# Optimization experiments

Measured on AMD Instinct MI355X. Metric: run time of the kernel, lower is better.

Reference implementation:

```python
import jax, jax.numpy as jnp
import numpy as np

B, T, H, NSPK = 8, 1024, 1024, 2
LN_EPS = 1e-5


def setup_inputs() -> dict:
    key = jax.random.key(0)
    ks = jax.random.split(key, 12)
    s = 1.0 / np.sqrt(H)
    return {
        "x": jax.random.normal(ks[0], (B, T, H), jnp.float32),
        "qmask": jax.random.uniform(ks[1], (B, T, NSPK), jnp.float32),
        "dia_len": jax.random.randint(ks[2], (B,), T // 2, T + 1),
        "wp": 8,
        "wf": 8,
        "W_msg": jax.random.normal(ks[3], (H, H), jnp.float32) * s,
        "b_msg": jax.random.normal(ks[4], (H,), jnp.float32) * s,
        "W_self": jax.random.normal(ks[5], (H, H), jnp.float32) * s,
        "b_self": jax.random.normal(ks[6], (H,), jnp.float32) * s,
        "W_out": jax.random.normal(ks[7], (H, H), jnp.float32) * s,
        "b_out": jax.random.normal(ks[8], (H,), jnp.float32) * s,
        "gamma": jnp.ones((H,), jnp.float32),
        "beta": jnp.zeros((H,), jnp.float32),
    }


def reference(x, qmask, dia_len, wp, wf, W_msg, b_msg, W_self, b_self, W_out, b_out, gamma, beta):
    Bb, Tt, Hh = x.shape
    spk = jnp.argmax(qmask, axis=-1)                     # [B,T]
    pos = jnp.arange(Tt)
    offs = jnp.arange(-wp, wf + 1)                       # [W]
    idx = pos[:, None] + offs[None, :]                   # [T,W] window indices
    vlen = dia_len[:, None, None]                        # [B,1,1]
    valid = (idx[None] >= 0) & (idx[None] <= vlen - 1)   # [B,T,W]
    idxc = jnp.clip(idx, 0, Tt - 1)
    nb = jnp.take(x, idxc, axis=1)                       # [B,T,W,H]
    nb_spk = jnp.take(spk, idxc, axis=1)                 # [B,T,W]
    same = (nb_spk == spk[:, :, None]).astype(x.dtype)
    w = jnp.where(valid, 0.5 + 0.5 * same, 0.0)          # speaker weights, masked
    cnt = jnp.maximum(valid.sum(-1).astype(x.dtype), 1.0)  # window sizes [B,T]
    msg = jnp.einsum('btw,btwh->bth', w, nb) / cnt[..., None]
    h = x @ W_self + b_self + msg @ W_msg + b_msg        # per-node fusion
    node_valid = (pos[None, :] < dia_len[:, None])[..., None]
    out = jnp.where(node_valid, h, x)                    # nodes past dia_len keep x
    y = jax.nn.relu(out) @ W_out + b_out                 # dropout = identity (eval)
    z = x + y
    mean = z.mean(-1, keepdims=True)
    var = z.var(-1, keepdims=True)
    return gamma * (z - mean) / jnp.sqrt(var + LN_EPS) + beta
```

## Files before the change

### kernel.cpp

```cpp
#include <hip/hip_runtime.h>


typedef unsigned short u16;
typedef float floatx4 __attribute__((ext_vector_type(4)));
typedef short shortx8 __attribute__((ext_vector_type(8)));

#define T_ 1024
#define H_ 1024

__device__ __forceinline__ float bf2f(u16 v) {
    return __uint_as_float(((unsigned)v) << 16);
}
__device__ __forceinline__ u16 f2bf(float f) {
    unsigned u = __float_as_uint(f);
    return (u16)((u + 0x7fffu + ((u >> 16) & 1u)) >> 16);
}
__device__ __forceinline__ void async16(const void* g, void* l) {
    __builtin_amdgcn_global_load_lds(
        (__attribute__((address_space(1))) void*)g,
        (__attribute__((address_space(3))) void*)l, 16, 0, 0);
}

__global__ __launch_bounds__(256)
void prep(const float* __restrict__ Wself, const float* __restrict__ Wmsg,
          const float* __restrict__ Wout, const float* __restrict__ x,
          u16* __restrict__ wt1, u16* __restrict__ wt_out, u16* __restrict__ xbf)
{
    __shared__ float s[32][33];
    const int bid = blockIdx.x;
    if (bid < 3072) {
        const int wid = bid >> 10;
        const int rem = bid & 1023;
        const float* src = (wid == 0) ? Wself : ((wid == 1) ? Wmsg : Wout);
        const int n0 = (rem & 31) * 32, k0 = (rem >> 5) * 32;
        const int tx = threadIdx.x & 31, ty = threadIdx.x >> 5;
#pragma unroll
        for (int i = 0; i < 4; ++i) {
            int k = k0 + ty + 8 * i;
            s[ty + 8 * i][tx] = src[(size_t)k * H_ + n0 + tx];
        }
        __syncthreads();
#pragma unroll
        for (int i = 0; i < 4; ++i) {
            int n = n0 + ty + 8 * i;
            u16 v = f2bf(s[tx][ty + 8 * i]);
            if (wid == 0)      wt1[(size_t)n * 1024 + k0 + tx] = v;
            else if (wid == 1) wt1[(size_t)(n + 1024) * 1024 + k0 + tx] = v;
            else               wt_out[(size_t)n * 1024 + k0 + tx] = v;
        }
    } else {
        const size_t i = ((size_t)(bid - 3072) * 256 + threadIdx.x) * 8;
        float4 v0 = *(const float4*)(x + i);
        float4 v1 = *(const float4*)(x + i + 4);
        ushort4 o0, o1;
        o0.x = f2bf(v0.x); o0.y = f2bf(v0.y); o0.z = f2bf(v0.z); o0.w = f2bf(v0.w);
        o1.x = f2bf(v1.x); o1.y = f2bf(v1.y); o1.z = f2bf(v1.z); o1.w = f2bf(v1.w);
        *(ushort4*)(xbf + i) = o0;
        *(ushort4*)(xbf + i + 4) = o1;
    }
}

template <int KLEN, int EPI>
__global__ __launch_bounds__(256)
void gemm_bt(const u16* __restrict__ A, const u16* __restrict__ Bt,
             u16* __restrict__ O0, u16* __restrict__ O1)
{
    __shared__ u16 smem[2 * 8192];
    const int tid = threadIdx.x;
    const int bn = blockIdx.x * 128;
    const int bm = blockIdx.y * 128;
    const int kb = blockIdx.z * KLEN;
    const int wave = tid >> 6, lane = tid & 63;
    const int wr = wave >> 1, wc = wave & 1;
    const int lrow = lane & 15, lq = lane >> 4;

    const int srow = tid >> 2;
    const int skc  = (tid & 3) ^ ((srow >> 1) & 3);
    const u16* gA0 = A + (size_t)(bm + srow) * 1024 + kb + skc * 8;
    const u16* gA1 = gA0 + (size_t)64 * 1024;
    const u16* gB0 = Bt + (size_t)(bn + srow) * 1024 + kb + skc * 8;
    const u16* gB1 = gB0 + (size_t)64 * 1024;

    floatx4 acc[4][4];
#pragma unroll
    for (int i = 0; i < 4; ++i)
#pragma unroll
        for (int j = 0; j < 4; ++j)
            acc[i][j] = (floatx4){0.f, 0.f, 0.f, 0.f};

    const int swz = (lrow >> 1) & 3;
    const int aoff = (wr * 64 + lrow) * 32 + ((lq ^ swz) * 8);
    const int boff = 4096 + (wc * 64 + lrow) * 32 + ((lq ^ swz) * 8);

    auto issue = [&](int s, int p) {
        u16* base = smem + p * 8192 + wave * 512;
        const int k = s * 32;
        async16(gA0 + k, base);
        async16(gA1 + k, base + 2048);
        async16(gB0 + k, base + 4096);
        async16(gB1 + k, base + 4096 + 2048);
    };

    constexpr int NS = KLEN / 32;
    issue(0, 0);
#pragma unroll 2
    for (int s = 0; s < NS; ++s) {
        const int p = s & 1;
        if (s + 1 < NS) {
            issue(s + 1, p ^ 1);
            asm volatile("s_waitcnt vmcnt(4)" ::: "memory");
        } else {
            asm volatile("s_waitcnt vmcnt(0)" ::: "memory");
        }
        asm volatile("s_barrier" ::: "memory");
        const u16* pa = smem + p * 8192 + aoff;
        const u16* pb = smem + p * 8192 + boff;
        shortx8 av[4], bv[4];
#pragma unroll
        for (int i = 0; i < 4; ++i) av[i] = *(const shortx8*)(pa + i * 512);
#pragma unroll
        for (int j = 0; j < 4; ++j) bv[j] = *(const shortx8*)(pb + j * 512);
#pragma unroll
        for (int i = 0; i < 4; ++i)
#pragma unroll
            for (int j = 0; j < 4; ++j)
                acc[i][j] = __builtin_amdgcn_mfma_f32_16x16x32_bf16(
                    av[i], bv[j], acc[i][j], 0, 0, 0);
        asm volatile("s_barrier" ::: "memory");
    }

    u16* O;
    int cbase;
    if (EPI == 0) { O = (bn < 1024) ? O0 : O1; cbase = bn & 1023; }
    else          { O = blockIdx.z ? O1 : O0;  cbase = bn; }
#pragma unroll
    for (int i = 0; i < 4; ++i) {
        const int row0 = bm + wr * 64 + i * 16 + lq * 4;
#pragma unroll
        for (int j = 0; j < 4; ++j) {
            const int col = cbase + wc * 64 + j * 16 + lrow;
#pragma unroll
            for (int r = 0; r < 4; ++r)
                O[(size_t)(row0 + r) * 1024 + col] = f2bf(acc[i][j][r]);
        }
    }
}

__global__ __launch_bounds__(256)
void combine(u16* __restrict__ uv, const u16* __restrict__ v,
             const float* __restrict__ x, const float* __restrict__ qmask,
             const int* __restrict__ dia_len, const float* __restrict__ b_self,
             const float* __restrict__ b_msg)
{
    const int t = blockIdx.x;
    const int b = blockIdx.y;
    const int tid = threadIdx.x;
    const int dlen = dia_len[b];
    const int c4 = tid * 4;
    const size_t rowg = (size_t)b * T_ + t;

    const float* qb = qmask + (size_t)b * T_ * 2;
    const int spk_t = (qb[t * 2 + 1] > qb[t * 2]) ? 1 : 0;

    float wts[17];
    int cnt = 0;
#pragma unroll
    for (int o = 0; o < 17; ++o) {
        const int idx = t + o - 8;
        if (idx >= 0 && idx < dlen) {
            ++cnt;
            const int spk_i = (qb[idx * 2 + 1] > qb[idx * 2]) ? 1 : 0;
            wts[o] = (spk_i == spk_t) ? 1.0f : 0.5f;
        } else {
            wts[o] = 0.0f;
        }
    }
    const float inv = 1.0f / (float)(cnt > 0 ? cnt : 1);

    float a0 = 0.f, a1 = 0.f, a2 = 0.f, a3 = 0.f;
#pragma unroll
    for (int o = 0; o < 17; ++o) {
        if (wts[o] != 0.0f) {
            const float w = wts[o] * inv;
            ushort4 vv = *(const ushort4*)(v + (rowg + (o - 8)) * 1024 + c4);
            a0 += w * bf2f(vv.x); a1 += w * bf2f(vv.y);
            a2 += w * bf2f(vv.z); a3 += w * bf2f(vv.w);
        }
    }

    float4 bs;
    {
        float4 b1 = *(const float4*)(b_self + c4);
        float4 b2 = *(const float4*)(b_msg + c4);
        bs.x = b1.x + b2.x; bs.y = b1.y + b2.y;
        bs.z = b1.z + b2.z; bs.w = b1.w + b2.w;
    }

    ushort4 u4 = *(const ushort4*)(uv + rowg * 1024 + c4);
    float4 xv = *(const float4*)(x + rowg * H_ + c4);
    const bool sel = (t < dlen);
    float h0 = bf2f(u4.x) + bs.x + a0;
    float h1 = bf2f(u4.y) + bs.y + a1;
    float h2 = bf2f(u4.z) + bs.z + a2;
    float h3 = bf2f(u4.w) + bs.w + a3;
    ushort4 outv;
    outv.x = f2bf(fmaxf(sel ? h0 : xv.x, 0.f));
    outv.y = f2bf(fmaxf(sel ? h1 : xv.y, 0.f));
    outv.z = f2bf(fmaxf(sel ? h2 : xv.z, 0.f));
    outv.w = f2bf(fmaxf(sel ? h3 : xv.w, 0.f));
    *(ushort4*)(uv + rowg * 1024 + c4) = outv;
}

__global__ __launch_bounds__(256)
void ln_final(const u16* __restrict__ P0, const u16* __restrict__ P1,
              const float* __restrict__ x, const float* __restrict__ b_out,
              const float* __restrict__ gamma, const float* __restrict__ beta,
              float* __restrict__ out)
{
    const int row = blockIdx.x;
    const int tid = threadIdx.x;
    const size_t base = (size_t)row * H_ + tid * 4;
    float4 xv = *(const float4*)(x + base);
    ushort4 p0 = *(const ushort4*)(P0 + base);
    ushort4 p1 = *(const ushort4*)(P1 + base);
    float4 bo = *(const float4*)(b_out + tid * 4);
    float4 v;
    v.x = xv.x + bf2f(p0.x) + bf2f(p1.x) + bo.x;
    v.y = xv.y + bf2f(p0.y) + bf2f(p1.y) + bo.y;
    v.z = xv.z + bf2f(p0.z) + bf2f(p1.z) + bo.z;
    v.w = xv.w + bf2f(p0.w) + bf2f(p1.w) + bo.w;
    float s = v.x + v.y + v.z + v.w;
    float q = v.x * v.x + v.y * v.y + v.z * v.z + v.w * v.w;
#pragma unroll
    for (int off = 32; off > 0; off >>= 1) {
        s += __shfl_down(s, off);
        q += __shfl_down(q, off);
    }
    __shared__ float ps[4], pq[4];
    const int wave = tid >> 6, lane = tid & 63;
    if (lane == 0) { ps[wave] = s; pq[wave] = q; }
    __syncthreads();
    const float S = ps[0] + ps[1] + ps[2] + ps[3];
    const float Q = pq[0] + pq[1] + pq[2] + pq[3];
    const float mean = S * (1.0f / 1024.0f);
    const float var = Q * (1.0f / 1024.0f) - mean * mean;
    const float inv = rsqrtf(var + 1e-5f);
    float4 g = *(const float4*)(gamma + tid * 4);
    float4 bt = *(const float4*)(beta + tid * 4);
    float4 o;
    o.x = g.x * (v.x - mean) * inv + bt.x;
    o.y = g.y * (v.y - mean) * inv + bt.y;
    o.z = g.z * (v.z - mean) * inv + bt.z;
    o.w = g.w * (v.w - mean) * inv + bt.w;
    *(float4*)(out + base) = o;
}

extern "C" void kernel_launch(void* const* d_in, const int* in_sizes, int n_in,
                              void* d_out, int out_size, void* d_ws, size_t ws_size,
                              hipStream_t stream)
{
    (void)in_sizes; (void)n_in; (void)out_size; (void)ws_size;
    const float* x       = (const float*)d_in[0];
    const float* qmask   = (const float*)d_in[1];
    const int*   dia_len = (const int*)d_in[2];
    const float* W_msg   = (const float*)d_in[5];
    const float* b_msg   = (const float*)d_in[6];
    const float* W_self  = (const float*)d_in[7];
    const float* b_self  = (const float*)d_in[8];
    const float* W_out   = (const float*)d_in[9];
    const float* b_out   = (const float*)d_in[10];
    const float* gamma   = (const float*)d_in[11];
    const float* beta    = (const float*)d_in[12];
    float* out = (float*)d_out;

    char* ws = (char*)d_ws;
    u16* region0 = (u16*)ws;
    u16* region1 = (u16*)(ws + (size_t)(16u << 20));
    u16* region2 = (u16*)(ws + (size_t)(32u << 20));
    u16* wt1     = (u16*)(ws + (size_t)(48u << 20));
    u16* wt_out  = (u16*)(ws + (size_t)(52u << 20));

    prep<<<dim3(7168), 256, 0, stream>>>(W_self, W_msg, W_out, x,
                                         wt1, wt_out, region0);
    gemm_bt<1024, 0><<<dim3(16, 64, 1), 256, 0, stream>>>(region0, wt1,
                                                          region1, region2);
    combine<<<dim3(T_, 8), 256, 0, stream>>>(region1, region2, x, qmask,
                                             dia_len, b_self, b_msg);
    gemm_bt<512, 1><<<dim3(8, 64, 2), 256, 0, stream>>>(region1, wt_out,
                                                        region2, region0);
    ln_final<<<dim3(8192), 256, 0, stream>>>(region2, region0, x, b_out,
                                             gamma, beta, out);
}
```

Baseline: 229.6 us.

## Use 32x32x16 MFMA with triple-buffered LDS and bf16 x in combine

The GEMM switches from 16x16x32 to 32x32x16 bf16 MFMA tiles (2x2 per wave) with new LDS offsets and output mapping. It moves to a three-stage LDS ring, which lets it drop the trailing barrier in each k-step. Separately, combine reads the bf16 copy of x instead of the fp32 x for rows past dia_len, halving that read traffic. The bf16 read adds rounding only on that passthrough path, which is fed to a bf16 output anyway. The single remaining barrier with a 3-buffer ring is meant to stay race-free because a buffer is only refilled two steps after it is read.

Measured after the change: 231.9 us. Within noise of the previous version (+1.0%).

```diff
diff --git a/kernel.cpp b/kernel.cpp
--- a/kernel.cpp
+++ b/kernel.cpp
@@ -2,7 +2,7 @@
 
 
 typedef unsigned short u16;
-typedef float floatx4 __attribute__((ext_vector_type(4)));
+typedef float floatx16 __attribute__((ext_vector_type(16)));
 typedef short shortx8 __attribute__((ext_vector_type(8)));
 
 #define T_ 1024
@@ -65,14 +65,14 @@
 void gemm_bt(const u16* __restrict__ A, const u16* __restrict__ Bt,
              u16* __restrict__ O0, u16* __restrict__ O1)
 {
-    __shared__ u16 smem[2 * 8192];
+    __shared__ u16 smem[3 * 8192];
     const int tid = threadIdx.x;
     const int bn = blockIdx.x * 128;
     const int bm = blockIdx.y * 128;
     const int kb = blockIdx.z * KLEN;
     const int wave = tid >> 6, lane = tid & 63;
     const int wr = wave >> 1, wc = wave & 1;
-    const int lrow = lane & 15, lq = lane >> 4;
+    const int l32 = lane & 31, hi = lane >> 5;
 
     const int srow = tid >> 2;
     const int skc  = (tid & 3) ^ ((srow >> 1) & 3);
@@ -81,19 +81,29 @@
     const u16* gB0 = Bt + (size_t)(bn + srow) * 1024 + kb + skc * 8;
     const u16* gB1 = gB0 + (size_t)64 * 1024;
 
-    floatx4 acc[4][4];
-#pragma unroll
-    for (int i = 0; i < 4; ++i)
-#pragma unroll
-        for (int j = 0; j < 4; ++j)
-            acc[i][j] = (floatx4){0.f, 0.f, 0.f, 0.f};
-
-    const int swz = (lrow >> 1) & 3;
-    const int aoff = (wr * 64 + lrow) * 32 + ((lq ^ swz) * 8);
-    const int boff = 4096 + (wc * 64 + lrow) * 32 + ((lq ^ swz) * 8);
-
-    auto issue = [&](int s, int p) {
-        u16* base = smem + p * 8192 + wave * 512;
+    floatx16 acc[2][2];
+#pragma unroll
+    for (int i = 0; i < 2; ++i)
+#pragma unroll
+        for (int j = 0; j < 2; ++j)
+#pragma unroll
+            for (int r = 0; r < 16; ++r)
+                acc[i][j][r] = 0.f;
+
+    int offA[2][2], offB[2][2];
+#pragma unroll
+    for (int i = 0; i < 2; ++i) {
+        const int rowA = wr * 64 + i * 32 + l32;
+        const int rowB = wc * 64 + i * 32 + l32;
+#pragma unroll
+        for (int s2 = 0; s2 < 2; ++s2) {
+            offA[i][s2] = rowA * 32 + (((2 * s2 + hi) ^ ((rowA >> 1) & 3)) * 8);
+            offB[i][s2] = 4096 + rowB * 32 + (((2 * s2 + hi) ^ ((rowB >> 1) & 3)) * 8);
+        }
+    }
+
+    auto issue = [&](int s, int q) {
+        u16* base = smem + q * 8192 + wave * 512;
         const int k = s * 32;
         async16(gA0 + k, base);
         async16(gA1 + k, base + 2048);
@@ -103,30 +113,34 @@
 
     constexpr int NS = KLEN / 32;
     issue(0, 0);
-#pragma unroll 2
+    int qr = 0;
     for (int s = 0; s < NS; ++s) {
-        const int p = s & 1;
         if (s + 1 < NS) {
-            issue(s + 1, p ^ 1);
+            const int qw = (qr == 2) ? 0 : qr + 1;
+            issue(s + 1, qw);
             asm volatile("s_waitcnt vmcnt(4)" ::: "memory");
         } else {
             asm volatile("s_waitcnt vmcnt(0)" ::: "memory");
         }
         asm volatile("s_barrier" ::: "memory");
-        const u16* pa = smem + p * 8192 + aoff;
-        const u16* pb = smem + p * 8192 + boff;
-        shortx8 av[4], bv[4];
-#pragma unroll
-        for (int i = 0; i < 4; ++i) av[i] = *(const shortx8*)(pa + i * 512);
-#pragma unroll
-        for (int j = 0; j < 4; ++j) bv[j] = *(const shortx8*)(pb + j * 512);
-#pragma unroll
-        for (int i = 0; i < 4; ++i)
-#pragma unroll
-            for (int j = 0; j < 4; ++j)
-                acc[i][j] = __builtin_amdgcn_mfma_f32_16x16x32_bf16(
-                    av[i], bv[j], acc[i][j], 0, 0, 0);
-        asm volatile("s_barrier" ::: "memory");
+        const u16* pb = smem + qr * 8192;
+        shortx8 av[2][2], bv[2][2];
+#pragma unroll
+        for (int i = 0; i < 2; ++i)
+#pragma unroll
+            for (int s2 = 0; s2 < 2; ++s2) {
+                av[i][s2] = *(const shortx8*)(pb + offA[i][s2]);
+                bv[i][s2] = *(const shortx8*)(pb + offB[i][s2]);
+            }
+#pragma unroll
+        for (int s2 = 0; s2 < 2; ++s2)
+#pragma unroll
+            for (int i = 0; i < 2; ++i)
+#pragma unroll
+                for (int j = 0; j < 2; ++j)
+                    acc[i][j] = __builtin_amdgcn_mfma_f32_32x32x16_bf16(
+                        av[i][s2], bv[j][s2], acc[i][j], 0, 0, 0);
+        qr = (qr == 2) ? 0 : qr + 1;
     }
 
     u16* O;
@@ -134,21 +148,23 @@
     if (EPI == 0) { O = (bn < 1024) ? O0 : O1; cbase = bn & 1023; }
     else          { O = blockIdx.z ? O1 : O0;  cbase = bn; }
 #pragma unroll
-    for (int i = 0; i < 4; ++i) {
-        const int row0 = bm + wr * 64 + i * 16 + lq * 4;
-#pragma unroll
-        for (int j = 0; j < 4; ++j) {
-            const int col = cbase + wc * 64 + j * 16 + lrow;
-#pragma unroll
-            for (int r = 0; r < 4; ++r)
-                O[(size_t)(row0 + r) * 1024 + col] = f2bf(acc[i][j][r]);
+    for (int i = 0; i < 2; ++i) {
+#pragma unroll
+        for (int j = 0; j < 2; ++j) {
+            const int col = cbase + wc * 64 + j * 32 + l32;
+#pragma unroll
+            for (int reg = 0; reg < 16; ++reg) {
+                const int row = bm + wr * 64 + i * 32 +
+                                (reg & 3) + 8 * (reg >> 2) + 4 * hi;
+                O[(size_t)row * 1024 + col] = f2bf(acc[i][j][reg]);
+            }
         }
     }
 }
 
 __global__ __launch_bounds__(256)
 void combine(u16* __restrict__ uv, const u16* __restrict__ v,
-             const float* __restrict__ x, const float* __restrict__ qmask,
+             const u16* __restrict__ xbf, const float* __restrict__ qmask,
              const int* __restrict__ dia_len, const float* __restrict__ b_self,
              const float* __restrict__ b_msg)
 {
@@ -197,17 +213,17 @@
     }
 
     ushort4 u4 = *(const ushort4*)(uv + rowg * 1024 + c4);
-    float4 xv = *(const float4*)(x + rowg * H_ + c4);
+    ushort4 xb = *(const ushort4*)(xbf + rowg * 1024 + c4);
     const bool sel = (t < dlen);
     float h0 = bf2f(u4.x) + bs.x + a0;
     float h1 = bf2f(u4.y) + bs.y + a1;
     float h2 = bf2f(u4.z) + bs.z + a2;
     float h3 = bf2f(u4.w) + bs.w + a3;
     ushort4 outv;
-    outv.x = f2bf(fmaxf(sel ? h0 : xv.x, 0.f));
-    outv.y = f2bf(fmaxf(sel ? h1 : xv.y, 0.f));
-    outv.z = f2bf(fmaxf(sel ? h2 : xv.z, 0.f));
-    outv.w = f2bf(fmaxf(sel ? h3 : xv.w, 0.f));
+    outv.x = f2bf(fmaxf(sel ? h0 : bf2f(xb.x), 0.f));
+    outv.y = f2bf(fmaxf(sel ? h1 : bf2f(xb.y), 0.f));
+    outv.z = f2bf(fmaxf(sel ? h2 : bf2f(xb.z), 0.f));
+    outv.w = f2bf(fmaxf(sel ? h3 : bf2f(xb.w), 0.f));
     *(ushort4*)(uv + rowg * 1024 + c4) = outv;
 }
 
@@ -284,7 +300,7 @@
                                          wt1, wt_out, region0);
     gemm_bt<1024, 0><<<dim3(16, 64, 1), 256, 0, stream>>>(region0, wt1,
                                                           region1, region2);
-    combine<<<dim3(T_, 8), 256, 0, stream>>>(region1, region2, x, qmask,
+    combine<<<dim3(T_, 8), 256, 0, stream>>>(region1, region2, region0, qmask,
                                              dia_len, b_self, b_msg);
     gemm_bt<512, 1><<<dim3(8, 64, 2), 256, 0, stream>>>(region1, wt_out,
                                                         region2, region0);
```
